# Performance work log

Hardware: AMD Instinct MI355X
Metric: run time of the kernel (lower is better)

The kernel has to match this reference:

```python
import jax, jax.numpy as jnp
import numpy as np

H = 16  # heads
D = 1024  # hidden
HD = D // H
FF = 4096
EPS = 1e-12


def _linear_params(key, d_in, d_out):
    k1, k2 = jax.random.split(key)
    bound = 1.0 / np.sqrt(d_in)
    W = jax.random.uniform(k1, (d_in, d_out), minval=-bound, maxval=bound, dtype=jnp.float32)
    b = jax.random.uniform(k2, (d_out,), minval=-bound, maxval=bound, dtype=jnp.float32)
    return W, b


def setup_inputs() -> dict:
    key = jax.random.key(0)
    ks = jax.random.split(key, 8)
    x = jax.random.normal(ks[0], (4, 2048, D), dtype=jnp.float32)
    mask = jnp.ones((4, 1, 1, 2048), dtype=jnp.int32)
    Wq, bq = _linear_params(ks[1], D, D)
    Wk, bk = _linear_params(ks[2], D, D)
    Wv, bv = _linear_params(ks[3], D, D)
    Wo, bo = _linear_params(ks[4], D, D)
    W1, b1 = _linear_params(ks[5], D, FF)
    W2, b2 = _linear_params(ks[6], FF, D)
    g1 = jnp.ones((D,), jnp.float32); be1 = jnp.zeros((D,), jnp.float32)
    g2 = jnp.ones((D,), jnp.float32); be2 = jnp.zeros((D,), jnp.float32)
    return {"x": x, "mask": mask,
            "Wq": Wq, "bq": bq, "Wk": Wk, "bk": bk, "Wv": Wv, "bv": bv,
            "Wo": Wo, "bo": bo, "W1": W1, "b1": b1, "W2": W2, "b2": b2,
            "g1": g1, "be1": be1, "g2": g2, "be2": be2}


def _layernorm(x, g, b):
    mu = jnp.mean(x, axis=-1, keepdims=True)
    var = jnp.mean(jnp.square(x - mu), axis=-1, keepdims=True)
    return (x - mu) / jnp.sqrt(var + EPS) * g + b


def reference(x, mask, Wq, bq, Wk, bk, Wv, bv, Wo, bo, W1, b1, W2, b2, g1, be1, g2, be2):
    B, L, _ = x.shape
    h = _layernorm(x, g1, be1)
    # [B, H, L, HD]
    q = (h @ Wq + bq).reshape(B, L, H, HD).transpose(0, 2, 1, 3)
    k = (h @ Wk + bk).reshape(B, L, H, HD).transpose(0, 2, 1, 3)
    v = (h @ Wv + bv).reshape(B, L, H, HD).transpose(0, 2, 1, 3)
    scores = jnp.einsum('bhqd,bhkd->bhqk', q, k) / np.sqrt(HD).astype(np.float32)
    scores = jnp.where(mask == 0, jnp.float32(-1e9), scores)
    attn = jax.nn.softmax(scores, axis=-1)  # dropout = identity (eval mode)
    out = jnp.einsum('bhqk,bhkd->bhqd', attn, v)
    out = out.transpose(0, 2, 1, 3).reshape(B, L, D)
    x = x + (out @ Wo + bo)
    h = _layernorm(x, g2, be2)
    ff = jax.nn.gelu(h @ W1 + b1, approximate=False) @ W2 + b2
    return x + ff
```

## Files before the change

kernel.cpp:

```cpp
#include <hip/hip_runtime.h>
#include <stdint.h>

#define D_MODEL 1024
#define NHEAD   16
#define HDIM    64
#define FFDIM   4096
#define BATCH   4
#define SEQ     2048
#define ROWS    (BATCH*SEQ)

typedef unsigned short u16;
typedef __bf16 bf16_t;
typedef bf16_t bf16x8 __attribute__((ext_vector_type(8)));
typedef float  f32x4  __attribute__((ext_vector_type(4)));

#define SCQ 0.18033688011112042f

__device__ __forceinline__ u16 f2bf(float f) {
  union { float f; unsigned u; } v; v.f = f;
  unsigned r = v.u + 0x7fffu + ((v.u >> 16) & 1u);
  return (u16)(r >> 16);
}

__device__ __forceinline__ void gl2lds16(const void* g, void* l) {
  __builtin_amdgcn_global_load_lds((const __attribute__((address_space(1))) void*)g,
                                   (__attribute__((address_space(3))) void*)l, 16, 0, 0);
}

#define MFMA_BF16(a, b, c) __builtin_amdgcn_mfma_f32_16x16x32_bf16((a), (b), (c), 0, 0, 0)
#define EXP2(x) __builtin_amdgcn_exp2f(x)

__global__ __launch_bounds__(256) void ln_kernel(const float* __restrict__ x,
                                                 const float* __restrict__ g,
                                                 const float* __restrict__ be,
                                                 u16* __restrict__ out) {
  __shared__ float red[10];
  int row = blockIdx.x;
  int t = threadIdx.x;
  const float* xr = x + (size_t)row * D_MODEL;
  float4 xv = ((const float4*)xr)[t];
  float s  = xv.x + xv.y + xv.z + xv.w;
  float s2 = xv.x*xv.x + xv.y*xv.y + xv.z*xv.z + xv.w*xv.w;
  for (int d = 32; d > 0; d >>= 1) { s += __shfl_down(s, d); s2 += __shfl_down(s2, d); }
  int wid = t >> 6;
  if ((t & 63) == 0) { red[wid*2] = s; red[wid*2+1] = s2; }
  __syncthreads();
  if (t == 0) {
    float a = 0.f, b2 = 0.f;
    for (int i = 0; i < 4; ++i) { a += red[i*2]; b2 += red[i*2+1]; }
    red[8] = a; red[9] = b2;
  }
  __syncthreads();
  float mu  = red[8] * (1.0f / D_MODEL);
  float var = red[9] * (1.0f / D_MODEL) - mu*mu;
  float rstd = rsqrtf(var + 1e-12f);
  float4 gv = ((const float4*)g)[t];
  float4 bv = ((const float4*)be)[t];
  unsigned long long o =
      (unsigned long long)f2bf((xv.x - mu) * rstd * gv.x + bv.x)
    | ((unsigned long long)f2bf((xv.y - mu) * rstd * gv.y + bv.y) << 16)
    | ((unsigned long long)f2bf((xv.z - mu) * rstd * gv.z + bv.z) << 32)
    | ((unsigned long long)f2bf((xv.w - mu) * rstd * gv.w + bv.w) << 48);
  ((unsigned long long*)out)[(size_t)row * (D_MODEL/4) + t] = o;
}

__global__ __launch_bounds__(256) void wt_kernel(const float* __restrict__ W,
                                                 u16* __restrict__ Wt, int K, int N) {
  __shared__ float tile[32][33];
  int n0 = blockIdx.x * 32, k0 = blockIdx.y * 32;
  int tx = threadIdx.x & 31, ty = threadIdx.x >> 5;
  #pragma unroll
  for (int i = 0; i < 4; ++i) {
    int k = ty + i*8;
    tile[k][tx] = W[(size_t)(k0 + k) * N + n0 + tx];
  }
  __syncthreads();
  #pragma unroll
  for (int i = 0; i < 4; ++i) {
    int n = ty + i*8;
    Wt[(size_t)(n0 + n) * K + k0 + tx] = f2bf(tile[tx][n]);
  }
}

__global__ __launch_bounds__(256) void vtrans_kernel(const u16* __restrict__ vb,
                                                     u16* __restrict__ vt) {
  __shared__ __align__(16) u16 tile[64][80];
  int kb = blockIdx.x * 64;
  int bh = blockIdx.y;
  int b = bh >> 4, h = bh & 15;
  int t = threadIdx.x;
  int key = t >> 2, dq = (t & 3) * 16;
  const u16* src = vb + (size_t)b*SEQ*D_MODEL + (size_t)(kb+key)*D_MODEL + h*HDIM + dq;
  *(bf16x8*)&tile[key][dq]     = *(const bf16x8*)(src);
  *(bf16x8*)&tile[key][dq + 8] = *(const bf16x8*)(src + 8);
  __syncthreads();
  int w = t >> 6, lane = t & 63;
  int kq = w * 16;
  u16 vals[16];
  #pragma unroll
  for (int e = 0; e < 16; ++e) vals[e] = tile[kq + e][lane];
  u16* dst = vt + (size_t)bh * HDIM * SEQ + (size_t)lane * SEQ + kb + kq;
  *(bf16x8*)dst       = *(const bf16x8*)&vals[0];
  *(bf16x8*)(dst + 8) = *(const bf16x8*)&vals[8];
}

__device__ __forceinline__ float gelu_f(float v) {
  return 0.5f * v * (1.0f + erff(v * 0.70710678118654752f));
}

template<int EPI>
__global__ __launch_bounds__(512, 2) void gemm256(const u16* __restrict__ A,
                                                  const u16* __restrict__ Bt,
                                                  const float* __restrict__ bias,
                                                  const float* __restrict__ resid,
                                                  void* __restrict__ outp,
                                                  int M, int N, int K,
                                                  const float* __restrict__ bias2,
                                                  const float* __restrict__ bias3,
                                                  void* __restrict__ out2,
                                                  void* __restrict__ out3) {
  __shared__ __align__(16) u16 sA[3][128*64];
  __shared__ __align__(16) u16 sB[3][256*64];
  const int tid = threadIdx.x;
  const int lane = tid & 63, w = tid >> 6;
  const int r = lane & 15, kg = lane >> 4, r7 = r & 7;
  const int wr = w >> 2, wc = w & 3;

  const int gx = gridDim.x;
  const int nwg = gx * gridDim.y;
  const int orig = blockIdx.y * gx + blockIdx.x;
  const int lid = (orig & 7) * (nwg >> 3) + (orig >> 3);
  const int bm = lid / gx, bn = lid % gx;

  const int NT = K >> 6;

  size_t offA[2], offB[4];
  #pragma unroll
  for (int u = 0; u < 2; ++u) {
    int slot = u*512 + tid;
    int row = slot >> 3, g = slot & 7;
    offA[u] = (size_t)(bm*128 + row) * K + ((g ^ (row & 7)) * 8);
  }
  #pragma unroll
  for (int u = 0; u < 4; ++u) {
    int slot = u*512 + tid;
    int row = slot >> 3, g = slot & 7;
    offB[u] = (size_t)(bn*256 + row) * K + ((g ^ (row & 7)) * 8);
  }

  f32x4 acc[4][4];
  #pragma unroll
  for (int m = 0; m < 4; ++m)
    #pragma unroll
    for (int n = 0; n < 4; ++n) acc[m][n] = f32x4{0.f, 0.f, 0.f, 0.f};

  const float* bsel = bias;
  u16* osel = (u16*)outp;
  int bnl = bn;
  float qscale = 1.0f;
  if (EPI == 3) {
    int sec = bn >> 2;
    bsel = (sec == 0) ? bias : (sec == 1 ? bias2 : bias3);
    osel = (u16*)((sec == 0) ? outp : (sec == 1 ? out2 : out3));
    if (sec == 0) qscale = SCQ;
    bnl = bn & 3;
  }
  float bv4[4];
  #pragma unroll
  for (int n = 0; n < 4; ++n) bv4[n] = bsel[bnl*256 + wc*64 + n*16 + r];

  #pragma unroll
  for (int u = 0; u < 2; ++u) gl2lds16(A  + offA[u],      &sA[0][(u*512+tid)*8]);
  #pragma unroll
  for (int u = 0; u < 4; ++u) gl2lds16(Bt + offB[u],      &sB[0][(u*512+tid)*8]);
  #pragma unroll
  for (int u = 0; u < 2; ++u) gl2lds16(A  + offA[u] + 64, &sA[1][(u*512+tid)*8]);
  #pragma unroll
  for (int u = 0; u < 4; ++u) gl2lds16(Bt + offB[u] + 64, &sB[1][(u*512+tid)*8]);
  asm volatile("s_waitcnt vmcnt(6)" ::: "memory");
  __builtin_amdgcn_s_barrier();

  int buf = 0;
  for (int t = 0; t < NT; ++t) {
    const bool pre = (t + 2 < NT);
    int nb = buf + 2; if (nb >= 3) nb -= 3;
    const size_t koff = (size_t)(t + 2) * 64;

    bf16x8 af0[4], bf0[4];
    #pragma unroll
    for (int m = 0; m < 4; ++m)
      af0[m] = *(const bf16x8*)&sA[buf][(wr*64 + m*16 + r)*64 + ((kg ^ r7) * 8)];
    #pragma unroll
    for (int n = 0; n < 4; ++n)
      bf0[n] = *(const bf16x8*)&sB[buf][(wc*64 + n*16 + r)*64 + ((kg ^ r7) * 8)];
    if (pre) {
      gl2lds16(A  + offA[0] + koff, &sA[nb][(0*512+tid)*8]);
      gl2lds16(A  + offA[1] + koff, &sA[nb][(1*512+tid)*8]);
      gl2lds16(Bt + offB[0] + koff, &sB[nb][(0*512+tid)*8]);
    }
    __builtin_amdgcn_s_barrier();
    asm volatile("s_waitcnt lgkmcnt(0)" ::: "memory");
    __builtin_amdgcn_s_setprio(1);
    #pragma unroll
    for (int m = 0; m < 4; ++m)
      #pragma unroll
      for (int n = 0; n < 4; ++n)
        acc[m][n] = MFMA_BF16(af0[m], bf0[n], acc[m][n]);
    __builtin_amdgcn_s_setprio(0);
    __builtin_amdgcn_s_barrier();

    bf16x8 af1[4], bf1[4];
    #pragma unroll
    for (int m = 0; m < 4; ++m)
      af1[m] = *(const bf16x8*)&sA[buf][(wr*64 + m*16 + r)*64 + (((4 + kg) ^ r7) * 8)];
    #pragma unroll
    for (int n = 0; n < 4; ++n)
      bf1[n] = *(const bf16x8*)&sB[buf][(wc*64 + n*16 + r)*64 + (((4 + kg) ^ r7) * 8)];
    if (pre) {
      gl2lds16(Bt + offB[1] + koff, &sB[nb][(1*512+tid)*8]);
      gl2lds16(Bt + offB[2] + koff, &sB[nb][(2*512+tid)*8]);
      gl2lds16(Bt + offB[3] + koff, &sB[nb][(3*512+tid)*8]);
    }
    __builtin_amdgcn_s_barrier();
    asm volatile("s_waitcnt lgkmcnt(0)" ::: "memory");
    __builtin_amdgcn_s_setprio(1);
    #pragma unroll
    for (int m = 0; m < 4; ++m)
      #pragma unroll
      for (int n = 0; n < 4; ++n)
        acc[m][n] = MFMA_BF16(af1[m], bf1[n], acc[m][n]);
    __builtin_amdgcn_s_setprio(0);
    if (pre) asm volatile("s_waitcnt vmcnt(6)" ::: "memory");
    else     asm volatile("s_waitcnt vmcnt(0)" ::: "memory");
    __builtin_amdgcn_s_barrier();
    buf += 1; if (buf >= 3) buf -= 3;
  }

  const int orow = bm*128 + wr*64;
  const int ocol = (EPI == 3 ? bnl : bn)*256 + wc*64;
  const int ostride = (EPI == 3) ? 1024 : N;
  #pragma unroll
  for (int m = 0; m < 4; ++m) {
    #pragma unroll
    for (int n = 0; n < 4; ++n) {
      #pragma unroll
      for (int j = 0; j < 4; ++j) {
        int rr = orow + m*16 + kg*4 + j;
        int cc = ocol + n*16 + r;
        size_t idx = (size_t)rr * ostride + cc;
        float v = acc[m][n][j] + bv4[n];
        if (EPI == 0)       ((u16*)outp)[idx]   = f2bf(v);
        else if (EPI == 1)  ((float*)outp)[idx] = resid[idx] + v;
        else if (EPI == 2)  ((u16*)outp)[idx]   = f2bf(gelu_f(v));
        else                osel[idx]           = f2bf(v * qscale);
      }
    }
  }
}

__global__ __launch_bounds__(256) void attn_kernel(const u16* __restrict__ qb,
                                                   const u16* __restrict__ kb,
                                                   const u16* __restrict__ vt,
                                                   const int* __restrict__ mask,
                                                   u16* __restrict__ ob) {
  __shared__ __align__(16) u16 sK[2][64*64];
  __shared__ __align__(16) u16 sV[2][64*64];
  __shared__ __align__(16) bf16_t sP[4][16*64];
  const float THR2 = 11.541560327111708f;
  int tid = threadIdx.x;
  int lane = tid & 63, w = tid >> 6;
  int r = lane & 15, kg = lane >> 4;
  int r7 = r & 7;
  int qt = blockIdx.x;
  int bh = blockIdx.y;
  int b = bh >> 4, h = bh & 15;
  size_t qkbase = (size_t)b * SEQ * D_MODEL + (size_t)h * HDIM;
  const u16* vtb = vt + (size_t)bh * HDIM * SEQ;
  const int* mrow = mask + b * SEQ;

  const u16* qrow = qb + qkbase + (size_t)(qt*64 + w*16 + r) * D_MODEL + kg*8;
  bf16x8 qf[2];
  qf[0] = *(const bf16x8*)(qrow);
  qf[1] = *(const bf16x8*)(qrow + 32);

  f32x4 oacc[4];
  #pragma unroll
  for (int n = 0; n < 4; ++n) oacc[n] = f32x4{0.f, 0.f, 0.f, 0.f};
  float m_run[4] = {-1e30f, -1e30f, -1e30f, -1e30f};
  float lsum[4]  = {0.f, 0.f, 0.f, 0.f};

  int ch0 = w*64 + lane, ch1 = ch0 + 256;
  int row0 = ch0 >> 3, col0 = ((ch0 & 7) ^ (row0 & 7)) * 8;
  int row1 = ch1 >> 3, col1 = ((ch1 & 7) ^ (row1 & 7)) * 8;
  const u16* kp0 = kb + qkbase + (size_t)row0 * D_MODEL + col0;
  const u16* kp1 = kb + qkbase + (size_t)row1 * D_MODEL + col1;
  const u16* vp0 = vtb + (size_t)row0 * SEQ + col0;
  const u16* vp1 = vtb + (size_t)row1 * SEQ + col1;

  const int NT = SEQ / 64;

  gl2lds16(kp0, &sK[0][ch0*8]);
  gl2lds16(kp1, &sK[0][ch1*8]);
  gl2lds16(vp0, &sV[0][ch0*8]);
  gl2lds16(vp1, &sV[0][ch1*8]);
  kp0 += 64*D_MODEL; kp1 += 64*D_MODEL; vp0 += 64; vp1 += 64;

  #pragma unroll 2
  for (int kt = 0; kt < NT; ++kt) {
    int cur = kt & 1;
    int key0 = kt * 64;
    if (kt + 1 < NT) {
      gl2lds16(kp0, &sK[cur^1][ch0*8]);
      gl2lds16(kp1, &sK[cur^1][ch1*8]);
      gl2lds16(vp0, &sV[cur^1][ch0*8]);
      gl2lds16(vp1, &sV[cur^1][ch1*8]);
      kp0 += 64*D_MODEL; kp1 += 64*D_MODEL; vp0 += 64; vp1 += 64;
      asm volatile("s_waitcnt vmcnt(4)" ::: "memory");
    } else {
      asm volatile("s_waitcnt vmcnt(0)" ::: "memory");
    }
    __builtin_amdgcn_s_barrier();

    const u16* Kt = sK[cur];
    const u16* Vt = sV[cur];

    f32x4 s[4];
    #pragma unroll
    for (int n = 0; n < 4; ++n) s[n] = f32x4{0.f, 0.f, 0.f, 0.f};
    #pragma unroll
    for (int c = 0; c < 2; ++c) {
      #pragma unroll
      for (int n = 0; n < 4; ++n) {
        bf16x8 kf = *(const bf16x8*)&Kt[(n*16 + r)*64 + (((c*4 + kg) ^ r7) * 8)];
        s[n] = MFMA_BF16(qf[c], kf, s[n]);
      }
    }

    int mk[4];
    #pragma unroll
    for (int n = 0; n < 4; ++n) mk[n] = mrow[key0 + n*16 + r];
    if (!__all((mk[0] & mk[1] & mk[2] & mk[3]) != 0)) {
      #pragma unroll
      for (int n = 0; n < 4; ++n)
        #pragma unroll
        for (int j = 0; j < 4; ++j)
          s[n][j] = mk[n] ? s[n][j] : -1e9f;
    }
    float tm[4];
    #pragma unroll
    for (int n = 0; n < 4; ++n)
      #pragma unroll
      for (int j = 0; j < 4; ++j)
        tm[j] = (n == 0) ? s[n][j] : fmaxf(tm[j], s[n][j]);

    bool grow = (tm[0] > m_run[0] + THR2) | (tm[1] > m_run[1] + THR2) |
                (tm[2] > m_run[2] + THR2) | (tm[3] > m_run[3] + THR2);
    if (__any(grow)) {
      #pragma unroll
      for (int d = 1; d < 16; d <<= 1) {
        #pragma unroll
        for (int j = 0; j < 4; ++j) tm[j] = fmaxf(tm[j], __shfl_xor(tm[j], d));
      }
      #pragma unroll
      for (int j = 0; j < 4; ++j) {
        float mn = fmaxf(m_run[j], tm[j]);
        float al = EXP2(m_run[j] - mn);
        m_run[j] = mn;
        lsum[j] *= al;
        oacc[0][j] *= al; oacc[1][j] *= al; oacc[2][j] *= al; oacc[3][j] *= al;
      }
    }
    bf16_t* pw = sP[w];
    #pragma unroll
    for (int n = 0; n < 4; ++n) {
      int cg = n*2 + (r >> 3);
      #pragma unroll
      for (int j = 0; j < 4; ++j) {
        float p = EXP2(s[n][j] - m_run[j]);
        lsum[j] += p;
        int row = kg*4 + j;
        pw[row*64 + ((cg ^ (row & 7)) * 8) + r7] = (bf16_t)p;
      }
    }
    bf16x8 pa[2];
    #pragma unroll
    for (int c = 0; c < 2; ++c)
      pa[c] = *(const bf16x8*)&sP[w][r*64 + (((c*4 + kg) ^ r7) * 8)];
    #pragma unroll
    for (int n = 0; n < 4; ++n) {
      #pragma unroll
      for (int c = 0; c < 2; ++c) {
        bf16x8 vf = *(const bf16x8*)&Vt[(n*16 + r)*64 + (((c*4 + kg) ^ r7) * 8)];
        oacc[n] = MFMA_BF16(pa[c], vf, oacc[n]);
      }
    }
    __builtin_amdgcn_s_barrier();
  }

  #pragma unroll
  for (int d = 1; d < 16; d <<= 1) {
    #pragma unroll
    for (int j = 0; j < 4; ++j) lsum[j] += __shfl_xor(lsum[j], d);
  }
  float rcp[4];
  #pragma unroll
  for (int j = 0; j < 4; ++j) rcp[j] = 1.0f / lsum[j];
  #pragma unroll
  for (int n = 0; n < 4; ++n) {
    #pragma unroll
    for (int j = 0; j < 4; ++j) {
      int q = qt*64 + w*16 + kg*4 + j;
      int d = h*HDIM + n*16 + r;
      ob[(size_t)(b*SEQ + q) * D_MODEL + d] = f2bf(oacc[n][j] * rcp[j]);
    }
  }
}

extern "C" void kernel_launch(void* const* d_in, const int* in_sizes, int n_in,
                              void* d_out, int out_size, void* d_ws, size_t ws_size,
                              hipStream_t stream) {
  const float* x   = (const float*)d_in[0];
  const int*  mask = (const int*)d_in[1];
  const float* Wq = (const float*)d_in[2];  const float* bq = (const float*)d_in[3];
  const float* Wk = (const float*)d_in[4];  const float* bk = (const float*)d_in[5];
  const float* Wv = (const float*)d_in[6];  const float* bv = (const float*)d_in[7];
  const float* Wo = (const float*)d_in[8];  const float* bo = (const float*)d_in[9];
  const float* W1 = (const float*)d_in[10]; const float* b1 = (const float*)d_in[11];
  const float* W2 = (const float*)d_in[12]; const float* b2 = (const float*)d_in[13];
  const float* g1 = (const float*)d_in[14]; const float* be1 = (const float*)d_in[15];
  const float* g2 = (const float*)d_in[16]; const float* be2 = (const float*)d_in[17];

  const size_t MB = 1u << 20;
  char* ws = (char*)d_ws;
  u16*  hln  = (u16*)(ws);
  u16*  vt   = (u16*)(ws);
  u16*  qb   = (u16*)(ws + 16*MB);
  u16*  kb   = (u16*)(ws + 32*MB);
  u16*  vb   = (u16*)(ws + 48*MB);
  u16*  attn = (u16*)(ws + 64*MB);
  u16*  ff1  = (u16*)(ws + 16*MB);
  float* x2  = (float*)(ws + 80*MB);
  u16*  WqkvT= (u16*)(ws + 112*MB);
  u16*  WqT  = WqkvT;
  u16*  WkT  = (u16*)(ws + 114*MB);
  u16*  WvT  = (u16*)(ws + 116*MB);
  u16*  WoT  = (u16*)(ws + 118*MB);
  u16*  W1T  = (u16*)(ws + 120*MB);
  u16*  W2T  = (u16*)(ws + 128*MB);

  dim3 tb(256);
  wt_kernel<<<dim3(1024/32, 1024/32), tb, 0, stream>>>(Wq, WqT, 1024, 1024);
  wt_kernel<<<dim3(1024/32, 1024/32), tb, 0, stream>>>(Wk, WkT, 1024, 1024);
  wt_kernel<<<dim3(1024/32, 1024/32), tb, 0, stream>>>(Wv, WvT, 1024, 1024);
  wt_kernel<<<dim3(1024/32, 1024/32), tb, 0, stream>>>(Wo, WoT, 1024, 1024);
  wt_kernel<<<dim3(4096/32, 1024/32), tb, 0, stream>>>(W1, W1T, 1024, 4096);
  wt_kernel<<<dim3(1024/32, 4096/32), tb, 0, stream>>>(W2, W2T, 4096, 1024);

  ln_kernel<<<ROWS, tb, 0, stream>>>(x, g1, be1, hln);

  dim3 gb(512);
  gemm256<3><<<dim3(3072/256, ROWS/128), gb, 0, stream>>>(hln, WqkvT, bq, nullptr, qb,
                                                          ROWS, 3072, 1024,
                                                          bk, bv, kb, vb);

  vtrans_kernel<<<dim3(SEQ/64, BATCH*NHEAD), tb, 0, stream>>>(vb, vt);

  attn_kernel<<<dim3(SEQ/64, BATCH*NHEAD), tb, 0, stream>>>(qb, kb, vt, mask, attn);

  gemm256<1><<<dim3(1024/256, ROWS/128), gb, 0, stream>>>(attn, WoT, bo, x, x2,
                                                          ROWS, 1024, 1024,
                                                          nullptr, nullptr, nullptr, nullptr);

  ln_kernel<<<ROWS, tb, 0, stream>>>(x2, g2, be2, hln);

  gemm256<2><<<dim3(4096/256, ROWS/128), gb, 0, stream>>>(hln, W1T, b1, nullptr, ff1,
                                                          ROWS, 4096, 1024,
                                                          nullptr, nullptr, nullptr, nullptr);

  gemm256<1><<<dim3(1024/256, ROWS/128), gb, 0, stream>>>(ff1, W2T, b2, x2, (float*)d_out,
                                                          ROWS, 1024, 4096,
                                                          nullptr, nullptr, nullptr, nullptr);
}
```

Baseline: 460.6 us.

## Software-pipeline LDS fragment loads with MFMA and drop per-half barriers

Restructures the GEMM main loop so that LDS fragment reads for the next k-half are issued while MFMAs run on the already-loaded fragments, with one workgroup barrier per k-tile instead of three. All global-to-LDS prefetches for the next tile are issued together up front. This is meant to hide LDS read latency behind matrix work and cut synchronisation overhead, at the cost of more live registers (two fragment sets) and a peeled epilogue iteration.

```diff
diff --git a/kernel.cpp b/kernel.cpp
--- a/kernel.cpp
+++ b/kernel.cpp
@@ -169,6 +169,24 @@
   #pragma unroll
   for (int n = 0; n < 4; ++n) bv4[n] = bsel[bnl*256 + wc*64 + n*16 + r];
 
+  auto load_frags = [&](bf16x8 (&aa)[4], bf16x8 (&bb)[4], int bbuf, int sl) {
+    #pragma unroll
+    for (int m = 0; m < 4; ++m)
+      aa[m] = *(const bf16x8*)&sA[bbuf][(wr*64 + m*16 + r)*64 + (((sl*4 + kg) ^ r7) * 8)];
+    #pragma unroll
+    for (int n = 0; n < 4; ++n)
+      bb[n] = *(const bf16x8*)&sB[bbuf][(wc*64 + n*16 + r)*64 + (((sl*4 + kg) ^ r7) * 8)];
+  };
+  auto mfma16 = [&](bf16x8 (&aa)[4], bf16x8 (&bb)[4]) {
+    __builtin_amdgcn_s_setprio(1);
+    #pragma unroll
+    for (int m = 0; m < 4; ++m)
+      #pragma unroll
+      for (int n = 0; n < 4; ++n)
+        acc[m][n] = MFMA_BF16(aa[m], bb[n], acc[m][n]);
+    __builtin_amdgcn_s_setprio(0);
+  };
+
   #pragma unroll
   for (int u = 0; u < 2; ++u) gl2lds16(A  + offA[u],      &sA[0][(u*512+tid)*8]);
   #pragma unroll
@@ -180,61 +198,39 @@
   asm volatile("s_waitcnt vmcnt(6)" ::: "memory");
   __builtin_amdgcn_s_barrier();
 
+  bf16x8 a0[4], b0[4], a1[4], b1[4];
+  load_frags(a0, b0, 0, 0);
+
   int buf = 0;
-  for (int t = 0; t < NT; ++t) {
+  for (int t = 0; t < NT - 1; ++t) {
+    int nb = buf + 2; if (nb >= 3) nb -= 3;
     const bool pre = (t + 2 < NT);
-    int nb = buf + 2; if (nb >= 3) nb -= 3;
     const size_t koff = (size_t)(t + 2) * 64;
 
-    bf16x8 af0[4], bf0[4];
-    #pragma unroll
-    for (int m = 0; m < 4; ++m)
-      af0[m] = *(const bf16x8*)&sA[buf][(wr*64 + m*16 + r)*64 + ((kg ^ r7) * 8)];
-    #pragma unroll
-    for (int n = 0; n < 4; ++n)
-      bf0[n] = *(const bf16x8*)&sB[buf][(wc*64 + n*16 + r)*64 + ((kg ^ r7) * 8)];
+    load_frags(a1, b1, buf, 1);
     if (pre) {
       gl2lds16(A  + offA[0] + koff, &sA[nb][(0*512+tid)*8]);
       gl2lds16(A  + offA[1] + koff, &sA[nb][(1*512+tid)*8]);
       gl2lds16(Bt + offB[0] + koff, &sB[nb][(0*512+tid)*8]);
-    }
-    __builtin_amdgcn_s_barrier();
-    asm volatile("s_waitcnt lgkmcnt(0)" ::: "memory");
-    __builtin_amdgcn_s_setprio(1);
-    #pragma unroll
-    for (int m = 0; m < 4; ++m)
-      #pragma unroll
-      for (int n = 0; n < 4; ++n)
-        acc[m][n] = MFMA_BF16(af0[m], bf0[n], acc[m][n]);
-    __builtin_amdgcn_s_setprio(0);
-    __builtin_amdgcn_s_barrier();
-
-    bf16x8 af1[4], bf1[4];
-    #pragma unroll
-    for (int m = 0; m < 4; ++m)
-      af1[m] = *(const bf16x8*)&sA[buf][(wr*64 + m*16 + r)*64 + (((4 + kg) ^ r7) * 8)];
-    #pragma unroll
-    for (int n = 0; n < 4; ++n)
-      bf1[n] = *(const bf16x8*)&sB[buf][(wc*64 + n*16 + r)*64 + (((4 + kg) ^ r7) * 8)];
-    if (pre) {
       gl2lds16(Bt + offB[1] + koff, &sB[nb][(1*512+tid)*8]);
       gl2lds16(Bt + offB[2] + koff, &sB[nb][(2*512+tid)*8]);
       gl2lds16(Bt + offB[3] + koff, &sB[nb][(3*512+tid)*8]);
     }
-    __builtin_amdgcn_s_barrier();
+    mfma16(a0, b0);
     asm volatile("s_waitcnt lgkmcnt(0)" ::: "memory");
-    __builtin_amdgcn_s_setprio(1);
-    #pragma unroll
-    for (int m = 0; m < 4; ++m)
-      #pragma unroll
-      for (int n = 0; n < 4; ++n)
-        acc[m][n] = MFMA_BF16(af1[m], bf1[n], acc[m][n]);
-    __builtin_amdgcn_s_setprio(0);
+    __builtin_amdgcn_sched_barrier(0);
     if (pre) asm volatile("s_waitcnt vmcnt(6)" ::: "memory");
     else     asm volatile("s_waitcnt vmcnt(0)" ::: "memory");
     __builtin_amdgcn_s_barrier();
-    buf += 1; if (buf >= 3) buf -= 3;
-  }
+
+    int bnext = buf + 1; if (bnext >= 3) bnext -= 3;
+    load_frags(a0, b0, bnext, 0);
+    mfma16(a1, b1);
+    buf = bnext;
+  }
+  load_frags(a1, b1, buf, 1);
+  mfma16(a0, b0);
+  mfma16(a1, b1);
 
   const int orow = bm*128 + wr*64;
   const int ocol = (EPI == 3 ? bnl : bn)*256 + wc*64;
```

Result: faster. 438.0 us (-4.9%).
